# Kernel tuning notes

Hardware: AMD Instinct MI355X
Metric: run time of the kernel (lower is better)

Reference implementation:

```python
import jax, jax.numpy as jnp
import numpy as np

NY, NU, NHIDDEN = 64, 64, 256
NHRZ, NBATCH = 1024, 128


def setup_inputs() -> dict:
    key = jax.random.key(0)
    ks = jax.random.split(key, 9)
    y0 = jax.random.normal(ks[0], (NBATCH, NY), dtype=jnp.float32)
    U = jax.random.normal(ks[1], (NHRZ, NBATCH, NU), dtype=jnp.float32)
    # parameters (match torch init: uniform(0,1) for continuous eigen params,
    # randn/sqrt(Nu) for B, Kaiming-uniform-ish for Linear layers)
    lmbd_cont_real = jax.random.uniform(ks[2], (NHIDDEN // 2,), dtype=jnp.float32)
    lmbd_cont_imag = jax.random.uniform(ks[3], (NHIDDEN // 2,), dtype=jnp.float32)
    B = jax.random.normal(ks[4], (NHIDDEN, NU), dtype=jnp.float32) / np.sqrt(NU)
    lim1 = 1.0 / np.sqrt(NY)
    W_y2x = jax.random.uniform(ks[5], (NHIDDEN, NY), dtype=jnp.float32, minval=-lim1, maxval=lim1)
    b_y2x = jax.random.uniform(ks[6], (NHIDDEN,), dtype=jnp.float32, minval=-lim1, maxval=lim1)
    lim2 = 1.0 / np.sqrt(NHIDDEN)
    W_x2y = jax.random.uniform(ks[7], (NY, NHIDDEN), dtype=jnp.float32, minval=-lim2, maxval=lim2)
    b_x2y = jax.random.uniform(ks[8], (NY,), dtype=jnp.float32, minval=-lim2, maxval=lim2)
    return {"y0": y0, "U": U, "lmbd_cont_real": lmbd_cont_real,
            "lmbd_cont_imag": lmbd_cont_imag, "B": B,
            "W_y2x": W_y2x, "b_y2x": b_y2x, "W_x2y": W_x2y, "b_x2y": b_x2y}


def reference(y0, U, lmbd_cont_real, lmbd_cont_imag, B, W_y2x, b_y2x, W_x2y, b_x2y):
    n = lmbd_cont_real.shape[0]  # Nhidden // 2
    r = jnp.exp(-jnp.abs(lmbd_cont_real))
    theta = (np.pi / 2.0) * lmbd_cont_imag
    lmbd_real = r * jnp.cos(theta)  # [n]
    lmbd_imag = r * jnp.sin(theta)  # [n]
    nf = jnp.sqrt(1.0 - jnp.exp(-2.0 * jnp.abs(lmbd_cont_real)))
    nf = jnp.concatenate([nf, nf])  # [Nhidden]
    # Bu[t,b,h] = (U @ B^T) * nf
    Bu = jnp.einsum('tbu,hu->tbh', U, B) * nf  # [Nhrz, Nbatch, Nhidden]
    x0 = y0 @ W_y2x.T + b_y2x  # [Nbatch, Nhidden]

    # x @ A^T with A = [[diag(lr), -diag(li)], [diag(li), diag(lr)]] is a
    # per-pair 2x2 rotation -> pure elementwise ops (same math, no dense matmul)
    def step(x, bu):
        x1, x2 = x[:, :n], x[:, n:]
        xn = jnp.concatenate([lmbd_real * x1 - lmbd_imag * x2,
                              lmbd_imag * x1 + lmbd_real * x2], axis=-1) + bu
        return xn, xn

    _, X = jax.lax.scan(step, x0, Bu)  # X: [Nhrz, Nbatch, Nhidden]
    Y = X @ W_x2y.T + b_x2y  # [Nhrz, Nbatch, Ny]
    return Y
```

## Files before the change

### kernel.cpp

```cpp
#include <hip/hip_runtime.h>
#include <stdint.h>

#define T_HRZ 1024
#define NBAT  128
#define NHID  256
#define NPAIR 128
#define NUIN  64
#define NYOUT 64
#define LCH   16
#define CCH   64

#define WS_LAM   0
#define WS_LAML  256
#define WS_X0P   512
#define WS_WBU   33280
#define WS_WBY   41472
#define WS_S     49664
#define WS_E     2146816

typedef __attribute__((ext_vector_type(8))) short short8;
typedef __attribute__((ext_vector_type(4))) float float4v;

__device__ __forceinline__ unsigned int f2bf_bits(float x) {
  unsigned int u = __float_as_uint(x);
  return (u + 0x7fffu + ((u >> 16) & 1u)) >> 16;
}

__global__ __launch_bounds__(256) void k_prep(
    const float* __restrict__ y0, const float* __restrict__ lrc,
    const float* __restrict__ lic, const float* __restrict__ Bm,
    const float* __restrict__ Wy2x, const float* __restrict__ by2x,
    const float* __restrict__ Wx2y, float* __restrict__ ws)
{
  int blk = blockIdx.x;
  int h = threadIdx.x;
  if (blk < NBAT) {
    __shared__ float y0s[NYOUT];
    if (h < NYOUT) y0s[h] = y0[blk * NYOUT + h];
    __syncthreads();
    float acc = by2x[h];
    const float* wr = Wy2x + h * NYOUT;
#pragma unroll 16
    for (int k = 0; k < NYOUT; ++k) acc += y0s[k] * wr[k];
    int j = h & (NPAIR - 1);
    int comp = h >> 7;
    ws[WS_X0P + (blk * NPAIR + j) * 2 + comp] = acc;
  } else if (blk == NBAT) {
    if (h < NPAIR) {
      float a  = fabsf(lrc[h]);
      float r  = expf(-a);
      float th = 1.5707963267948966f * lic[h];
      float lr = r * cosf(th);
      float li = r * sinf(th);
      ws[WS_LAM + h]         = lr;
      ws[WS_LAM + NPAIR + h] = li;
      float pr = lr, pi_ = li;
      for (int l = 1; l < LCH; ++l) {
        float nr = pr * lr - pi_ * li;
        float ni = pr * li + pi_ * lr;
        pr = nr; pi_ = ni;
      }
      ws[WS_LAML + h]         = pr;
      ws[WS_LAML + NPAIR + h] = pi_;
    }
  } else if (blk == NBAT + 1) {
    unsigned short* wbu = (unsigned short*)(ws + WS_WBU);
    for (int idx = h; idx < 16384; idx += 256) {
      int nt   = idx >> 10;
      int kk   = (idx >> 9) & 1;
      int lane = (idx >> 3) & 63;
      int jj   = idx & 7;
      int u  = kk * 32 + (lane >> 4) * 8 + jj;
      int hh = nt * 16 + (lane & 15);
      float a2 = fabsf(lrc[hh & (NPAIR - 1)]);
      float nf = sqrtf(1.f - expf(-2.f * a2));
      wbu[idx] = (unsigned short)f2bf_bits(Bm[hh * NUIN + u] * nf);
    }
  } else {
    unsigned short* wby = (unsigned short*)(ws + WS_WBY);
    for (int idx = h; idx < 16384; idx += 256) {
      int nt   = idx >> 12;
      int kk   = (idx >> 9) & 7;
      int lane = (idx >> 3) & 63;
      int jj   = idx & 7;
      int hh = kk * 32 + (lane >> 4) * 8 + jj;
      int y  = nt * 16 + (lane & 15);
      wby[idx] = (unsigned short)f2bf_bits(Wx2y[y * NHID + hh]);
    }
  }
}

__global__ __launch_bounds__(128) void k_phaseA(
    const float* __restrict__ U, float* __restrict__ ws)
{
  int c = blockIdx.x, b = blockIdx.y;
  int tid = threadIdx.x, wave = tid >> 6, lane = tid & 63;
  int m = lane & 15, quad = lane >> 4;
  __shared__ float X32[LCH * 260];

  const float* urow = U + ((size_t)(c * LCH + m) * NBAT + b) * NUIN;
  short8 afr[2];
#pragma unroll
  for (int kk = 0; kk < 2; ++kk) {
    int u0 = kk * 32 + quad * 8;
    float4 va = *(const float4*)(urow + u0);
    float4 vb = *(const float4*)(urow + u0 + 4);
    short8 f;
    f[0] = (short)f2bf_bits(va.x); f[1] = (short)f2bf_bits(va.y);
    f[2] = (short)f2bf_bits(va.z); f[3] = (short)f2bf_bits(va.w);
    f[4] = (short)f2bf_bits(vb.x); f[5] = (short)f2bf_bits(vb.y);
    f[6] = (short)f2bf_bits(vb.z); f[7] = (short)f2bf_bits(vb.w);
    afr[kk] = f;
  }

  const short8* wbu = (const short8*)(ws + WS_WBU);
  float4v z = {0.f, 0.f, 0.f, 0.f};
  float4v acc[8];
#pragma unroll
  for (int n = 0; n < 8; ++n) acc[n] = z;
#pragma unroll
  for (int n = 0; n < 8; ++n) {
    int nt = wave * 8 + n;
    acc[n] = __builtin_amdgcn_mfma_f32_16x16x32_bf16(afr[0], wbu[(nt * 2 + 0) * 64 + lane], acc[n], 0, 0, 0);
    acc[n] = __builtin_amdgcn_mfma_f32_16x16x32_bf16(afr[1], wbu[(nt * 2 + 1) * 64 + lane], acc[n], 0, 0, 0);
  }

#pragma unroll
  for (int n = 0; n < 8; ++n) {
    int hh = (wave * 8 + n) * 16 + (lane & 15);
#pragma unroll
    for (int r = 0; r < 4; ++r)
      X32[(quad * 4 + r) * 260 + hh] = acc[n][r];
  }
  __syncthreads();

  int j = tid;
  float lr = ws[WS_LAM + j], li = ws[WS_LAM + NPAIR + j];
  float s1 = 0.f, s2 = 0.f;
#pragma unroll
  for (int l = 0; l < LCH; ++l) {
    float v1 = X32[l * 260 + j];
    float v2 = X32[l * 260 + NPAIR + j];
    float n1 = lr * s1 - li * s2 + v1;
    float n2 = li * s1 + lr * s2 + v2;
    s1 = n1; s2 = n2;
  }
  ((float2*)(ws + WS_S))[((size_t)c * NBAT + b) * NPAIR + j] = make_float2(s1, s2);
}

__global__ __launch_bounds__(128) void k_phaseB(float* __restrict__ ws)
{
  int b = blockIdx.x, j = threadIdx.x;
  float e1 = ws[WS_X0P + (b * NPAIR + j) * 2 + 0];
  float e2 = ws[WS_X0P + (b * NPAIR + j) * 2 + 1];
  float Lr = ws[WS_LAML + j], Li = ws[WS_LAML + NPAIR + j];
  const float2* sp = (const float2*)(ws + WS_S);
  float2* ep = (float2*)(ws + WS_E);
  const size_t cs = (size_t)NBAT * NPAIR;
  size_t o0 = (size_t)b * NPAIR + j;
  float2 buf[8];
#pragma unroll
  for (int k = 0; k < 8; ++k) buf[k] = sp[k * cs + o0];
  for (int g = 0; g < 8; ++g) {
    float2 nxt[8];
    if (g < 7) {
#pragma unroll
      for (int k = 0; k < 8; ++k) nxt[k] = sp[(size_t)((g + 1) * 8 + k) * cs + o0];
    }
#pragma unroll
    for (int k = 0; k < 8; ++k) {
      ep[(size_t)(g * 8 + k) * cs + o0] = make_float2(e1, e2);
      float n1 = Lr * e1 - Li * e2 + buf[k].x;
      float n2 = Li * e1 + Lr * e2 + buf[k].y;
      e1 = n1; e2 = n2;
    }
    if (g < 7) {
#pragma unroll
      for (int k = 0; k < 8; ++k) buf[k] = nxt[k];
    }
  }
}

__global__ __launch_bounds__(128) void k_phaseC(
    const float* __restrict__ U, const float* __restrict__ bx2y,
    float* __restrict__ out, float* __restrict__ ws)
{
  int c = blockIdx.x, b = blockIdx.y;
  int tid = threadIdx.x, wave = tid >> 6, lane = tid & 63;
  int m = lane & 15, quad = lane >> 4;
  __shared__ float X32[LCH * 260];
  __shared__ unsigned short XA[8 * 64 * 8];

  const float* urow = U + ((size_t)(c * LCH + m) * NBAT + b) * NUIN;
  short8 afr[2];
#pragma unroll
  for (int kk = 0; kk < 2; ++kk) {
    int u0 = kk * 32 + quad * 8;
    float4 va = *(const float4*)(urow + u0);
    float4 vb = *(const float4*)(urow + u0 + 4);
    short8 f;
    f[0] = (short)f2bf_bits(va.x); f[1] = (short)f2bf_bits(va.y);
    f[2] = (short)f2bf_bits(va.z); f[3] = (short)f2bf_bits(va.w);
    f[4] = (short)f2bf_bits(vb.x); f[5] = (short)f2bf_bits(vb.y);
    f[6] = (short)f2bf_bits(vb.z); f[7] = (short)f2bf_bits(vb.w);
    afr[kk] = f;
  }

  const short8* wbu = (const short8*)(ws + WS_WBU);
  float4v z = {0.f, 0.f, 0.f, 0.f};
  {
    float4v acc[8];
#pragma unroll
    for (int n = 0; n < 8; ++n) acc[n] = z;
#pragma unroll
    for (int n = 0; n < 8; ++n) {
      int nt = wave * 8 + n;
      acc[n] = __builtin_amdgcn_mfma_f32_16x16x32_bf16(afr[0], wbu[(nt * 2 + 0) * 64 + lane], acc[n], 0, 0, 0);
      acc[n] = __builtin_amdgcn_mfma_f32_16x16x32_bf16(afr[1], wbu[(nt * 2 + 1) * 64 + lane], acc[n], 0, 0, 0);
    }
#pragma unroll
    for (int n = 0; n < 8; ++n) {
      int hh = (wave * 8 + n) * 16 + (lane & 15);
#pragma unroll
      for (int r = 0; r < 4; ++r)
        X32[(quad * 4 + r) * 260 + hh] = acc[n][r];
    }
  }
  __syncthreads();

  int j = tid;
  float lr = ws[WS_LAM + j], li = ws[WS_LAM + NPAIR + j];
  float2 e = ((const float2*)(ws + WS_E))[((size_t)c * NBAT + b) * NPAIR + j];
  float x1 = e.x, x2 = e.y;
  int h1 = j, h2 = j + NPAIR;
  int base1 = ((h1 >> 5) << 9) + (((h1 >> 3) & 3) << 7) + (h1 & 7);
  int base2 = ((h2 >> 5) << 9) + (((h2 >> 3) & 3) << 7) + (h2 & 7);
#pragma unroll
  for (int l = 0; l < LCH; ++l) {
    float v1 = X32[l * 260 + j];
    float v2 = X32[l * 260 + NPAIR + j];
    float n1 = lr * x1 - li * x2 + v1;
    float n2 = li * x1 + lr * x2 + v2;
    x1 = n1; x2 = n2;
    XA[base1 + l * 8] = (unsigned short)f2bf_bits(x1);
    XA[base2 + l * 8] = (unsigned short)f2bf_bits(x2);
  }
  __syncthreads();

  const short8* xa = (const short8*)XA;
  const short8* wby = (const short8*)(ws + WS_WBY);
  float4v acc0 = z, acc1 = z;
  int nt0 = wave * 2, nt1 = nt0 + 1;
#pragma unroll
  for (int kk = 0; kk < 8; ++kk) {
    short8 a = xa[kk * 64 + lane];
    acc0 = __builtin_amdgcn_mfma_f32_16x16x32_bf16(a, wby[(nt0 * 8 + kk) * 64 + lane], acc0, 0, 0, 0);
    acc1 = __builtin_amdgcn_mfma_f32_16x16x32_bf16(a, wby[(nt1 * 8 + kk) * 64 + lane], acc1, 0, 0, 0);
  }

  int col = lane & 15;
  float bias0 = bx2y[nt0 * 16 + col];
  float bias1 = bx2y[nt1 * 16 + col];
#pragma unroll
  for (int r = 0; r < 4; ++r) {
    int row = quad * 4 + r;
    size_t o = ((size_t)(c * LCH + row) * NBAT + b) * NYOUT;
    out[o + nt0 * 16 + col] = acc0[r] + bias0;
    out[o + nt1 * 16 + col] = acc1[r] + bias1;
  }
}

extern "C" void kernel_launch(void* const* d_in, const int* in_sizes, int n_in,
                              void* d_out, int out_size, void* d_ws, size_t ws_size,
                              hipStream_t stream) {
  (void)in_sizes; (void)n_in; (void)out_size; (void)ws_size;
  const float* y0   = (const float*)d_in[0];
  const float* U    = (const float*)d_in[1];
  const float* lrc  = (const float*)d_in[2];
  const float* lic  = (const float*)d_in[3];
  const float* Bm   = (const float*)d_in[4];
  const float* Wy2x = (const float*)d_in[5];
  const float* by2x = (const float*)d_in[6];
  const float* Wx2y = (const float*)d_in[7];
  const float* bx2y = (const float*)d_in[8];
  float* out = (float*)d_out;
  float* ws  = (float*)d_ws;

  k_prep<<<dim3(NBAT + 3), 256, 0, stream>>>(y0, lrc, lic, Bm, Wy2x, by2x, Wx2y, ws);
  k_phaseA<<<dim3(CCH, NBAT), 128, 0, stream>>>(U, ws);
  k_phaseB<<<dim3(NBAT), 128, 0, stream>>>(ws);
  k_phaseC<<<dim3(CCH, NBAT), 128, 0, stream>>>(U, bx2y, out, ws);
}
```

Before: 167.7 us.

## Use bf16 interleaved LDS staging, padded XA layout, and batch-major grid order

Phases A and C now stage the Bu tile in LDS as bf16, interleaving each pair (h, h+128) into one 32-bit word and loading all 16 timesteps up front. The XA A-operand buffer gains padded strides to reduce LDS bank conflicts, and fp32-to-bf16 packing uses the hardware packed conversion. The grid is swapped so batch is the fast-varying block index, which makes consecutive blocks read contiguous U rows, and launch bounds are raised to ask for higher occupancy. Rounding Bu to bf16 before the recurrence adds precision loss that compounds over the scan.

Result: faster. 154.3 us (-8.0%).

```diff
diff --git a/kernel.cpp b/kernel.cpp
--- a/kernel.cpp
+++ b/kernel.cpp
@@ -1,4 +1,5 @@
 #include <hip/hip_runtime.h>
+#include <hip/hip_bf16.h>
 #include <stdint.h>
 
 #define T_HRZ 1024
@@ -18,12 +19,23 @@
 #define WS_S     49664
 #define WS_E     2146816
 
+#define X16_PITCH 264
+#define XA_SB 136
+#define XA_SK 552
+
 typedef __attribute__((ext_vector_type(8))) short short8;
 typedef __attribute__((ext_vector_type(4))) float float4v;
+
+union Frag { short8 s8; unsigned int u32[4]; };
 
 __device__ __forceinline__ unsigned int f2bf_bits(float x) {
   unsigned int u = __float_as_uint(x);
   return (u + 0x7fffu + ((u >> 16) & 1u)) >> 16;
+}
+
+__device__ __forceinline__ unsigned int pkbf(float a, float b) {
+  __hip_bfloat162 h = __float22bfloat162_rn(make_float2(a, b));
+  union { __hip_bfloat162 h2; unsigned int u; } cv; cv.h2 = h; return cv.u;
 }
 
 __global__ __launch_bounds__(256) void k_prep(
@@ -90,27 +102,25 @@
   }
 }
 
-__global__ __launch_bounds__(128) void k_phaseA(
+__global__ __launch_bounds__(128, 6) void k_phaseA(
     const float* __restrict__ U, float* __restrict__ ws)
 {
-  int c = blockIdx.x, b = blockIdx.y;
+  int b = blockIdx.x, c = blockIdx.y;
   int tid = threadIdx.x, wave = tid >> 6, lane = tid & 63;
-  int m = lane & 15, quad = lane >> 4;
-  __shared__ float X32[LCH * 260];
-
-  const float* urow = U + ((size_t)(c * LCH + m) * NBAT + b) * NUIN;
-  short8 afr[2];
+  int l15 = lane & 15, q = lane >> 4;
+  __shared__ unsigned short X16[LCH * X16_PITCH];
+
+  const float* urow = U + ((size_t)(c * LCH + l15) * NBAT + b) * NUIN;
+  Frag afr[2];
 #pragma unroll
   for (int kk = 0; kk < 2; ++kk) {
-    int u0 = kk * 32 + quad * 8;
+    int u0 = kk * 32 + q * 8;
     float4 va = *(const float4*)(urow + u0);
     float4 vb = *(const float4*)(urow + u0 + 4);
-    short8 f;
-    f[0] = (short)f2bf_bits(va.x); f[1] = (short)f2bf_bits(va.y);
-    f[2] = (short)f2bf_bits(va.z); f[3] = (short)f2bf_bits(va.w);
-    f[4] = (short)f2bf_bits(vb.x); f[5] = (short)f2bf_bits(vb.y);
-    f[6] = (short)f2bf_bits(vb.z); f[7] = (short)f2bf_bits(vb.w);
-    afr[kk] = f;
+    afr[kk].u32[0] = pkbf(va.x, va.y);
+    afr[kk].u32[1] = pkbf(va.z, va.w);
+    afr[kk].u32[2] = pkbf(vb.x, vb.y);
+    afr[kk].u32[3] = pkbf(vb.z, vb.w);
   }
 
   const short8* wbu = (const short8*)(ws + WS_WBU);
@@ -121,26 +131,31 @@
 #pragma unroll
   for (int n = 0; n < 8; ++n) {
     int nt = wave * 8 + n;
-    acc[n] = __builtin_amdgcn_mfma_f32_16x16x32_bf16(afr[0], wbu[(nt * 2 + 0) * 64 + lane], acc[n], 0, 0, 0);
-    acc[n] = __builtin_amdgcn_mfma_f32_16x16x32_bf16(afr[1], wbu[(nt * 2 + 1) * 64 + lane], acc[n], 0, 0, 0);
+    acc[n] = __builtin_amdgcn_mfma_f32_16x16x32_bf16(afr[0].s8, wbu[(nt * 2 + 0) * 64 + lane], acc[n], 0, 0, 0);
+    acc[n] = __builtin_amdgcn_mfma_f32_16x16x32_bf16(afr[1].s8, wbu[(nt * 2 + 1) * 64 + lane], acc[n], 0, 0, 0);
   }
 
 #pragma unroll
   for (int n = 0; n < 8; ++n) {
-    int hh = (wave * 8 + n) * 16 + (lane & 15);
+    int hh = (wave * 8 + n) * 16 + l15;
+    int off = (hh & 127) * 2 + (hh >> 7);
 #pragma unroll
     for (int r = 0; r < 4; ++r)
-      X32[(quad * 4 + r) * 260 + hh] = acc[n][r];
+      X16[(q * 4 + r) * X16_PITCH + off] = (unsigned short)f2bf_bits(acc[n][r]);
   }
   __syncthreads();
 
   int j = tid;
   float lr = ws[WS_LAM + j], li = ws[WS_LAM + NPAIR + j];
+  unsigned int pk[LCH];
+#pragma unroll
+  for (int l = 0; l < LCH; ++l)
+    pk[l] = *(const unsigned int*)(X16 + l * X16_PITCH + j * 2);
   float s1 = 0.f, s2 = 0.f;
 #pragma unroll
   for (int l = 0; l < LCH; ++l) {
-    float v1 = X32[l * 260 + j];
-    float v2 = X32[l * 260 + NPAIR + j];
+    float v1 = __uint_as_float(pk[l] << 16);
+    float v2 = __uint_as_float(pk[l] & 0xffff0000u);
     float n1 = lr * s1 - li * s2 + v1;
     float n2 = li * s1 + lr * s2 + v2;
     s1 = n1; s2 = n2;
@@ -181,29 +196,31 @@
   }
 }
 
-__global__ __launch_bounds__(128) void k_phaseC(
+__global__ __launch_bounds__(128, 4) void k_phaseC(
     const float* __restrict__ U, const float* __restrict__ bx2y,
     float* __restrict__ out, float* __restrict__ ws)
 {
-  int c = blockIdx.x, b = blockIdx.y;
+  int b = blockIdx.x, c = blockIdx.y;
   int tid = threadIdx.x, wave = tid >> 6, lane = tid & 63;
-  int m = lane & 15, quad = lane >> 4;
-  __shared__ float X32[LCH * 260];
-  __shared__ unsigned short XA[8 * 64 * 8];
-
-  const float* urow = U + ((size_t)(c * LCH + m) * NBAT + b) * NUIN;
-  short8 afr[2];
+  int l15 = lane & 15, q = lane >> 4;
+  __shared__ unsigned short X16[LCH * X16_PITCH];
+  __shared__ unsigned short XA[8 * XA_SK];
+
+  int j = tid;
+  float lr = ws[WS_LAM + j], li = ws[WS_LAM + NPAIR + j];
+  float2 e = ((const float2*)(ws + WS_E))[((size_t)c * NBAT + b) * NPAIR + j];
+
+  const float* urow = U + ((size_t)(c * LCH + l15) * NBAT + b) * NUIN;
+  Frag afr[2];
 #pragma unroll
   for (int kk = 0; kk < 2; ++kk) {
-    int u0 = kk * 32 + quad * 8;
+    int u0 = kk * 32 + q * 8;
     float4 va = *(const float4*)(urow + u0);
     float4 vb = *(const float4*)(urow + u0 + 4);
-    short8 f;
-    f[0] = (short)f2bf_bits(va.x); f[1] = (short)f2bf_bits(va.y);
-    f[2] = (short)f2bf_bits(va.z); f[3] = (short)f2bf_bits(va.w);
-    f[4] = (short)f2bf_bits(vb.x); f[5] = (short)f2bf_bits(vb.y);
-    f[6] = (short)f2bf_bits(vb.z); f[7] = (short)f2bf_bits(vb.w);
-    afr[kk] = f;
+    afr[kk].u32[0] = pkbf(va.x, va.y);
+    afr[kk].u32[1] = pkbf(va.z, va.w);
+    afr[kk].u32[2] = pkbf(vb.x, vb.y);
+    afr[kk].u32[3] = pkbf(vb.z, vb.w);
   }
 
   const short8* wbu = (const short8*)(ws + WS_WBU);
@@ -215,30 +232,32 @@
 #pragma unroll
     for (int n = 0; n < 8; ++n) {
       int nt = wave * 8 + n;
-      acc[n] = __builtin_amdgcn_mfma_f32_16x16x32_bf16(afr[0], wbu[(nt * 2 + 0) * 64 + lane], acc[n], 0, 0, 0);
-      acc[n] = __builtin_amdgcn_mfma_f32_16x16x32_bf16(afr[1], wbu[(nt * 2 + 1) * 64 + lane], acc[n], 0, 0, 0);
+      acc[n] = __builtin_amdgcn_mfma_f32_16x16x32_bf16(afr[0].s8, wbu[(nt * 2 + 0) * 64 + lane], acc[n], 0, 0, 0);
+      acc[n] = __builtin_amdgcn_mfma_f32_16x16x32_bf16(afr[1].s8, wbu[(nt * 2 + 1) * 64 + lane], acc[n], 0, 0, 0);
     }
 #pragma unroll
     for (int n = 0; n < 8; ++n) {
-      int hh = (wave * 8 + n) * 16 + (lane & 15);
+      int hh = (wave * 8 + n) * 16 + l15;
+      int off = (hh & 127) * 2 + (hh >> 7);
 #pragma unroll
       for (int r = 0; r < 4; ++r)
-        X32[(quad * 4 + r) * 260 + hh] = acc[n][r];
+        X16[(q * 4 + r) * X16_PITCH + off] = (unsigned short)f2bf_bits(acc[n][r]);
     }
   }
   __syncthreads();
 
-  int j = tid;
-  float lr = ws[WS_LAM + j], li = ws[WS_LAM + NPAIR + j];
-  float2 e = ((const float2*)(ws + WS_E))[((size_t)c * NBAT + b) * NPAIR + j];
+  unsigned int pk[LCH];
+#pragma unroll
+  for (int l = 0; l < LCH; ++l)
+    pk[l] = *(const unsigned int*)(X16 + l * X16_PITCH + j * 2);
+
+  int base1 = (j >> 5) * XA_SK       + ((j >> 3) & 3) * XA_SB + (j & 7);
+  int base2 = ((j >> 5) + 4) * XA_SK + ((j >> 3) & 3) * XA_SB + (j & 7);
   float x1 = e.x, x2 = e.y;
-  int h1 = j, h2 = j + NPAIR;
-  int base1 = ((h1 >> 5) << 9) + (((h1 >> 3) & 3) << 7) + (h1 & 7);
-  int base2 = ((h2 >> 5) << 9) + (((h2 >> 3) & 3) << 7) + (h2 & 7);
 #pragma unroll
   for (int l = 0; l < LCH; ++l) {
-    float v1 = X32[l * 260 + j];
-    float v2 = X32[l * 260 + NPAIR + j];
+    float v1 = __uint_as_float(pk[l] << 16);
+    float v2 = __uint_as_float(pk[l] & 0xffff0000u);
     float n1 = lr * x1 - li * x2 + v1;
     float n2 = li * x1 + lr * x2 + v2;
     x1 = n1; x2 = n2;
@@ -247,26 +266,24 @@
   }
   __syncthreads();
 
-  const short8* xa = (const short8*)XA;
   const short8* wby = (const short8*)(ws + WS_WBY);
   float4v acc0 = z, acc1 = z;
   int nt0 = wave * 2, nt1 = nt0 + 1;
 #pragma unroll
   for (int kk = 0; kk < 8; ++kk) {
-    short8 a = xa[kk * 64 + lane];
+    short8 a = *(const short8*)(XA + kk * XA_SK + q * XA_SB + l15 * 8);
     acc0 = __builtin_amdgcn_mfma_f32_16x16x32_bf16(a, wby[(nt0 * 8 + kk) * 64 + lane], acc0, 0, 0, 0);
     acc1 = __builtin_amdgcn_mfma_f32_16x16x32_bf16(a, wby[(nt1 * 8 + kk) * 64 + lane], acc1, 0, 0, 0);
   }
 
-  int col = lane & 15;
-  float bias0 = bx2y[nt0 * 16 + col];
-  float bias1 = bx2y[nt1 * 16 + col];
+  float bias0 = bx2y[nt0 * 16 + l15];
+  float bias1 = bx2y[nt1 * 16 + l15];
 #pragma unroll
   for (int r = 0; r < 4; ++r) {
-    int row = quad * 4 + r;
+    int row = q * 4 + r;
     size_t o = ((size_t)(c * LCH + row) * NBAT + b) * NYOUT;
-    out[o + nt0 * 16 + col] = acc0[r] + bias0;
-    out[o + nt1 * 16 + col] = acc1[r] + bias1;
+    out[o + nt0 * 16 + l15] = acc0[r] + bias0;
+    out[o + nt1 * 16 + l15] = acc1[r] + bias1;
   }
 }
 
@@ -287,7 +304,7 @@
   float* ws  = (float*)d_ws;
 
   k_prep<<<dim3(NBAT + 3), 256, 0, stream>>>(y0, lrc, lic, Bm, Wy2x, by2x, Wx2y, ws);
-  k_phaseA<<<dim3(CCH, NBAT), 128, 0, stream>>>(U, ws);
+  k_phaseA<<<dim3(NBAT, CCH), 128, 0, stream>>>(U, ws);
   k_phaseB<<<dim3(NBAT), 128, 0, stream>>>(ws);
-  k_phaseC<<<dim3(CCH, NBAT), 128, 0, stream>>>(U, bx2y, out, ws);
-}
+  k_phaseC<<<dim3(NBAT, CCH), 128, 0, stream>>>(U, bx2y, out, ws);
+}
```
